# Optimization experiments

Hardware: AMD Instinct MI355X
Metric: run time of the kernel (lower is better)

Reference implementation:

```python
import jax, jax.numpy as jnp
import numpy as np

BATCH = 64
ORIGINAL_DIM = 524288
PROJ_DIM = 8192
C = 4


def setup_inputs() -> dict:
    key = jax.random.key(0)
    k1, k2, k3 = jax.random.split(key, 3)
    x = jax.random.normal(k1, (BATCH, ORIGINAL_DIM), dtype=jnp.float32)
    rand_indices = jax.random.randint(k2, (ORIGINAL_DIM, C), 0, PROJ_DIM, dtype=jnp.int32)
    rand_signs = jax.random.randint(k3, (ORIGINAL_DIM, C), 0, 2, dtype=jnp.int32)
    return {"x": x, "rand_indices": rand_indices, "rand_signs": rand_signs}


def reference(x, rand_indices, rand_signs):
    # SJLT: out[b, rand_indices[d, j]] += x[b, d] * sign[d, j], scaled by 1/sqrt(c)
    B, D = x.shape
    c = rand_indices.shape[1]
    signs = (2 * rand_signs - 1).astype(x.dtype)  # {0,1} -> {-1,+1}
    scale = 1.0 / jnp.sqrt(jnp.asarray(c, dtype=x.dtype))
    out = jnp.zeros((B, PROJ_DIM), dtype=x.dtype)
    for j in range(c):  # small fixed loop over non-zeros per column
        out = out.at[:, rand_indices[:, j]].add(x * signs[:, j])
    return out * scale
```

## Files before the change

### kernel.cpp

```cpp
#include <hip/hip_runtime.h>


constexpr int BATCH = 64;
constexpr int DIM   = 524288;
constexpr int PROJ  = 8192;
constexpr int NENT  = DIM * 4;
constexpr int CAP   = 384;
constexpr int CSTR  = 388;

constexpr int NBLKA = 256;
constexpr int EPB   = NENT / NBLKA;
constexpr int NHB   = 512;
constexpr int HBP   = PROJ / NHB;
constexpr int CAPH  = 4608;
constexpr int TBLK  = 2048;
constexpr int MAXR  = 5;

__device__ __forceinline__ uint32_t f2bf(float f) {
    uint32_t u = __float_as_uint(f);
    return (u + 0x7fffu + ((u >> 16) & 1u)) >> 16;
}

__global__ __launch_bounds__(1024) void prep_kernel(
    const float* __restrict__ x, const int4* __restrict__ idx4,
    const int4* __restrict__ sgn4, uint32_t* __restrict__ gBase,
    uint32_t* __restrict__ dense, uint32_t* __restrict__ xT)
{
    __shared__ uint32_t sh[10260];
    const int t = threadIdx.x;

    if (blockIdx.x < NBLKA) {
        uint32_t* cntL    = sh;
        uint32_t* offL    = sh + 512;
        uint32_t* curL    = sh + 1024;
        uint32_t* wsum    = sh + 1536;
        uint32_t* gb      = sh + 1544;
        uint32_t* staging = sh + 2056;
        const int lane = t & 63;
        const int blk  = blockIdx.x;

        if (t < NHB) cntL[t] = 0;
        __syncthreads();

        int4 iv[2], sv[2];
        int  dd[2];
#pragma unroll
        for (int j = 0; j < 2; ++j) {
            int d = blk * 2048 + j * 1024 + t;
            dd[j] = d;
            iv[j] = idx4[d];
            sv[j] = sgn4[d];
        }
#pragma unroll
        for (int j = 0; j < 2; ++j) {
            atomicAdd(&cntL[(uint32_t)iv[j].x >> 4], 1u);
            atomicAdd(&cntL[(uint32_t)iv[j].y >> 4], 1u);
            atomicAdd(&cntL[(uint32_t)iv[j].z >> 4], 1u);
            atomicAdd(&cntL[(uint32_t)iv[j].w >> 4], 1u);
        }
        __syncthreads();
        uint32_t v = 0, s = 0;
        if (t < NHB) {
            s = cntL[t]; v = s;
#pragma unroll
            for (int off = 1; off < 64; off <<= 1) {
                uint32_t u = __shfl_up(v, off);
                if (lane >= off) v += u;
            }
            if (lane == 63) wsum[t >> 6] = v;
        }
        __syncthreads();
        if (t < NHB) {
            uint32_t wb = 0;
            for (int w0 = 0; w0 < (t >> 6); ++w0) wb += wsum[w0];
            uint32_t ex = wb + v - s;
            offL[t] = ex;
            curL[t] = ex;
        }
        __syncthreads();
#pragma unroll
        for (int j = 0; j < 2; ++j) {
            const uint32_t dv = (uint32_t)dd[j] << 1;
            int p, ss;
            uint32_t b, sl;
            p = iv[j].x; ss = sv[j].x & 1; b = (uint32_t)p >> 4;
            sl = atomicAdd(&curL[b], 1u);
            staging[sl] = ((uint32_t)(p & 15) << 20) | dv | (uint32_t)ss;
            p = iv[j].y; ss = sv[j].y & 1; b = (uint32_t)p >> 4;
            sl = atomicAdd(&curL[b], 1u);
            staging[sl] = ((uint32_t)(p & 15) << 20) | dv | (uint32_t)ss;
            p = iv[j].z; ss = sv[j].z & 1; b = (uint32_t)p >> 4;
            sl = atomicAdd(&curL[b], 1u);
            staging[sl] = ((uint32_t)(p & 15) << 20) | dv | (uint32_t)ss;
            p = iv[j].w; ss = sv[j].w & 1; b = (uint32_t)p >> 4;
            sl = atomicAdd(&curL[b], 1u);
            staging[sl] = ((uint32_t)(p & 15) << 20) | dv | (uint32_t)ss;
        }
        __syncthreads();
        if (t < NHB) gb[t] = atomicAdd(&gBase[t], cntL[t]);
        __syncthreads();
        const int w = t >> 6;
        for (int i = 0; i < NHB / 16; ++i) {
            const int b = w * (NHB / 16) + i;
            const uint32_t c   = cntL[b];
            const uint32_t src = offL[b];
            const uint32_t g0  = gb[b];
            const uint32_t lim = (g0 < (uint32_t)CAPH) ? ((uint32_t)CAPH - g0) : 0u;
            const uint32_t cw  = c < lim ? c : lim;
            uint32_t* dst = dense + (size_t)b * CAPH + g0;
            for (uint32_t j2 = lane; j2 < cw; j2 += 64) dst[j2] = staging[src + j2];
        }
    } else {
        float* tile = reinterpret_cast<float*>(sh);
        const int blk   = blockIdx.x - NBLKA;
        const int dbase = blk * 256;
        const int c  = t & 15;
        const int r  = t >> 4;
        const int a  = t & 15;
        const int dr = t >> 4;
#pragma unroll
        for (int it = 0; it < 4; ++it) {
            const int d0 = dbase + it * 64;
            float4 v = *reinterpret_cast<const float4*>(
                &x[(size_t)r * DIM + d0 + 4 * c]);
            __syncthreads();
            tile[r * 65 + 4 * c + 0] = v.x;
            tile[r * 65 + 4 * c + 1] = v.y;
            tile[r * 65 + 4 * c + 2] = v.z;
            tile[r * 65 + 4 * c + 3] = v.w;
            __syncthreads();
            uint32_t lo, hi;
            lo = f2bf(tile[(4 * a + 0) * 65 + dr] * 0.5f);
            hi = f2bf(tile[(4 * a + 1) * 65 + dr] * 0.5f);
            const uint32_t w0 = lo | (hi << 16);
            lo = f2bf(tile[(4 * a + 2) * 65 + dr] * 0.5f);
            hi = f2bf(tile[(4 * a + 3) * 65 + dr] * 0.5f);
            const uint32_t w1 = lo | (hi << 16);
            uint2 wv; wv.x = w0; wv.y = w1;
            *reinterpret_cast<uint2*>(&xT[(size_t)(d0 + dr) * 32 + 2 * a]) = wv;
        }
    }
}

__global__ __launch_bounds__(1024) void gather8_kernel(
    const uint32_t* __restrict__ dense, const uint32_t* __restrict__ gBase,
    const uint32_t* __restrict__ xT, float* __restrict__ out)
{
    __shared__ uint32_t csr[16 * CSTR];
    __shared__ uint32_t wcnt[16][16];
    __shared__ uint32_t baseL[16][16];
    __shared__ uint32_t cntF[16];
    __shared__ float    obuf[64][17];
    const int t    = threadIdx.x;
    const int w    = t >> 6;
    const int lane = t & 63;
    const int hb   = blockIdx.x;

    uint32_t nt = gBase[hb];
    if (nt > (uint32_t)CAPH) nt = (uint32_t)CAPH;
    const uint32_t* src = dense + (size_t)hb * CAPH;
    const uint32_t s0 = (nt * (uint32_t)w) >> 4;
    const uint32_t s1 = (nt * (uint32_t)(w + 1)) >> 4;

    uint32_t pay[MAXR];
    uint32_t c16[16];
#pragma unroll
    for (int q = 0; q < 16; ++q) c16[q] = 0;
#pragma unroll
    for (int r = 0; r < MAXR; ++r) {
        const uint32_t i2 = s0 + (uint32_t)(r * 64 + lane);
        const bool ok = i2 < s1;
        pay[r] = ok ? src[i2] : 0xFFFFFFFFu;
        const uint32_t pv = ok ? ((pay[r] >> 20) & 15u) : 99u;
#pragma unroll
        for (int q = 0; q < 16; ++q) {
            const unsigned long long m = __ballot(pv == (uint32_t)q);
            c16[q] += (uint32_t)__popcll(m);
        }
    }
    if (lane == 0) {
#pragma unroll
        for (int q = 0; q < 16; ++q) wcnt[w][q] = c16[q];
    }
    __syncthreads();
    if (t < 256) {
        const int w2 = t >> 4, q2 = t & 15;
        uint32_t acc = 0;
        for (int wp = 0; wp < w2; ++wp) acc += wcnt[wp][q2];
        baseL[w2][q2] = (uint32_t)(q2 * CSTR) + acc;
        if (w2 == 15) cntF[q2] = acc + wcnt[15][q2];
    }
    __syncthreads();
    uint32_t rb[16];
#pragma unroll
    for (int q = 0; q < 16; ++q) rb[q] = baseL[w][q];
    const unsigned long long below = ((unsigned long long)1 << lane) - 1ull;
#pragma unroll
    for (int r = 0; r < MAXR; ++r) {
        const uint32_t i2 = s0 + (uint32_t)(r * 64 + lane);
        const bool ok = i2 < s1;
        const uint32_t pv = ok ? ((pay[r] >> 20) & 15u) : 99u;
        uint32_t slot = 0xFFFFFFFFu;
#pragma unroll
        for (int q = 0; q < 16; ++q) {
            const unsigned long long m = __ballot(pv == (uint32_t)q);
            if (pv == (uint32_t)q) slot = rb[q] + (uint32_t)__popcll(m & below);
            rb[q] += (uint32_t)__popcll(m);
        }
        if (slot < (uint32_t)(16 * CSTR)) csr[slot] = pay[r] & 0xFFFFFu;
    }
    __syncthreads();

    const int half = lane >> 5;
    const int k    = lane & 31;
    const uint32_t n = cntF[w];
    const uint32_t* e = &csr[w * CSTR];
    float acc0 = 0.f, acc1 = 0.f;
    uint32_t base = 0;
    for (; base + 8 <= n; base += 8) {
        uint32_t e8[8];
#pragma unroll
        for (int q = 0; q < 8; ++q) e8[q] = e[base + q];
#pragma unroll
        for (int q = 0; q < 8; q += 2) {
            uint32_t sel = half ? e8[q + 1] : e8[q];
            uint32_t u = xT[(size_t)(sel >> 1) * 32 + k];
            u ^= (sel & 1u) ? 0u : 0x80008000u;
            acc0 += __uint_as_float(u << 16);
            acc1 += __uint_as_float(u & 0xffff0000u);
        }
    }
    for (; base < n; base += 2) {
        uint32_t eA = e[base];
        uint32_t eB = (base + 1 < n) ? e[base + 1] : 0u;
        uint32_t sel   = half ? eB : eA;
        bool     valid = (base + (uint32_t)half) < n;
        uint32_t u = 0u;
        if (valid) {
            u = xT[(size_t)(sel >> 1) * 32 + k];
            u ^= (sel & 1u) ? 0u : 0x80008000u;
        }
        acc0 += __uint_as_float(u << 16);
        acc1 += __uint_as_float(u & 0xffff0000u);
    }
    acc0 += __shfl_xor(acc0, 32);
    acc1 += __shfl_xor(acc1, 32);
    if (half == 0) {
        obuf[2 * k + 0][w] = acc0;
        obuf[2 * k + 1][w] = acc1;
    }
    __syncthreads();
    if (t < 256) {
        const int b = t >> 2, q = t & 3;
        float4 vv;
        vv.x = obuf[b][4 * q + 0];
        vv.y = obuf[b][4 * q + 1];
        vv.z = obuf[b][4 * q + 2];
        vv.w = obuf[b][4 * q + 3];
        *reinterpret_cast<float4*>(
            &out[(size_t)b * PROJ + hb * HBP + 4 * q]) = vv;
    }
}

__device__ __forceinline__ void lds_fadd(uint32_t byte_addr, float v) {
    asm volatile("ds_add_f32 %0, %1" :: "v"(byte_addr), "v"(v) : "memory");
}
__device__ __forceinline__ void lds_fadd_off32k(uint32_t byte_addr, float v) {
    asm volatile("ds_add_f32 %0, %1 offset:32768" :: "v"(byte_addr), "v"(v) : "memory");
}

__global__ __launch_bounds__(1024) void sjlt_scatter(
    const float* __restrict__ x, const int4* __restrict__ idx4,
    const int4* __restrict__ sgn4, float* __restrict__ out)
{
    __shared__ float acc[4 * PROJ];
    for (int i = threadIdx.x; i < 4 * PROJ; i += 1024) acc[i] = 0.0f;
    __syncthreads();
    const int row0 = blockIdx.y * 4;
    const int dbeg = blockIdx.x * (DIM / 16);
    const uint32_t accBase = (uint32_t)(uintptr_t)(&acc[0]);
    const float* xr0 = x + (size_t)(row0 + 0) * DIM;
    const float* xr1 = x + (size_t)(row0 + 1) * DIM;
    const float* xr2 = x + (size_t)(row0 + 2) * DIM;
    const float* xr3 = x + (size_t)(row0 + 3) * DIM;
    for (int d = dbeg + (int)threadIdx.x; d < dbeg + DIM / 16; d += 1024) {
        const int4 iv = idx4[d];
        const int4 sv = sgn4[d];
        const uint32_t u0 = __float_as_uint(xr0[d]);
        const uint32_t u1 = __float_as_uint(xr1[d]);
        const uint32_t u2 = __float_as_uint(xr2[d]);
        const uint32_t u3 = __float_as_uint(xr3[d]);
        const int p[4] = {iv.x, iv.y, iv.z, iv.w};
        const int s[4] = {sv.x, sv.y, sv.z, sv.w};
#pragma unroll
        for (int j = 0; j < 4; ++j) {
            const uint32_t flip = (uint32_t)(s[j] ^ 1) << 31;
            const uint32_t a01  = accBase + ((uint32_t)p[j] << 2);
            const uint32_t a23  = a01 + 2u * 32768u;
            lds_fadd        (a01, __uint_as_float(u0 ^ flip));
            lds_fadd_off32k (a01, __uint_as_float(u1 ^ flip));
            lds_fadd        (a23, __uint_as_float(u2 ^ flip));
            lds_fadd_off32k (a23, __uint_as_float(u3 ^ flip));
        }
    }
    __syncthreads();
    for (int i = threadIdx.x; i < 4 * PROJ; i += 1024) {
        const int r  = i >> 13;
        const int pp = i & (PROJ - 1);
        unsafeAtomicAdd(&out[(size_t)(row0 + r) * PROJ + pp], acc[i] * 0.5f);
    }
}

extern "C" void kernel_launch(void* const* d_in, const int* in_sizes, int n_in,
                              void* d_out, int out_size, void* d_ws, size_t ws_size,
                              hipStream_t stream) {
    const float* x   = (const float*)d_in[0];
    const int4*  idx = (const int4*) d_in[1];
    const int4*  sgn = (const int4*) d_in[2];
    float*       out = (float*)d_out;

    const size_t need_r13 = ((size_t)NHB + (size_t)NHB * CAPH + (size_t)DIM * 32) * 4;

    if (ws_size >= need_r13) {
        uint32_t* gBase = (uint32_t*)d_ws;
        uint32_t* dense = gBase + NHB;
        uint32_t* xT    = dense + (size_t)NHB * CAPH;

        hipMemsetAsync(gBase, 0, NHB * sizeof(uint32_t), stream);
        prep_kernel   <<<NBLKA + TBLK, 1024, 0, stream>>>(
            x, idx, sgn, gBase, dense, xT);
        gather8_kernel<<<NHB,          1024, 0, stream>>>(dense, gBase, xT, out);
    } else {
        hipMemsetAsync(d_out, 0, (size_t)out_size * sizeof(float), stream);
        dim3 grid(16, 16);
        sjlt_scatter<<<grid, 1024, 0, stream>>>(x, idx, sgn, out);
    }
}
```

Measured before the change: 309.9 us.

## Replace in-block CSR bucketing with per-wave register accumulators and tree reduction

The gather kernel no longer sorts each block's entries into 16 per-column CSR buckets in LDS using ballots and prefix sums. Each wave now walks its own slice of entries directly and adds every value into one of 16 register accumulators, picked by a wave-uniform switch on the column id. The waves' partial sums are then combined with a log-depth tree reduction through LDS. This removes the two ballot passes and the CSR build, but uses many more registers, runs half the lanes idle, and adds several barrier rounds for the reduction. It also relies on every entry a wave reads in one step having the same column id, since readfirstlane takes the first lane's value.

```diff
diff --git a/kernel.cpp b/kernel.cpp
--- a/kernel.cpp
+++ b/kernel.cpp
@@ -5,16 +5,12 @@
 constexpr int DIM   = 524288;
 constexpr int PROJ  = 8192;
 constexpr int NENT  = DIM * 4;
-constexpr int CAP   = 384;
-constexpr int CSTR  = 388;
-
 constexpr int NBLKA = 256;
 constexpr int EPB   = NENT / NBLKA;
 constexpr int NHB   = 512;
 constexpr int HBP   = PROJ / NHB;
 constexpr int CAPH  = 4608;
 constexpr int TBLK  = 2048;
-constexpr int MAXR  = 5;
 
 __device__ __forceinline__ uint32_t f2bf(float f) {
     uint32_t u = __float_as_uint(f);
@@ -142,123 +138,94 @@
     }
 }
 
-__global__ __launch_bounds__(1024) void gather8_kernel(
+#define G9_CASE(Q) case Q: acc0[Q] += v0; acc1[Q] += v1; break;
+#define G9_SWITCH(PV)                                                     \
+    switch (PV) {                                                         \
+        G9_CASE(0)  G9_CASE(1)  G9_CASE(2)  G9_CASE(3)                    \
+        G9_CASE(4)  G9_CASE(5)  G9_CASE(6)  G9_CASE(7)                    \
+        G9_CASE(8)  G9_CASE(9)  G9_CASE(10) G9_CASE(11)                   \
+        G9_CASE(12) G9_CASE(13) G9_CASE(14) G9_CASE(15)                   \
+        default: break;                                                   \
+    }
+
+__global__ __launch_bounds__(1024) void gather9_kernel(
     const uint32_t* __restrict__ dense, const uint32_t* __restrict__ gBase,
     const uint32_t* __restrict__ xT, float* __restrict__ out)
 {
-    __shared__ uint32_t csr[16 * CSTR];
-    __shared__ uint32_t wcnt[16][16];
-    __shared__ uint32_t baseL[16][16];
-    __shared__ uint32_t cntF[16];
-    __shared__ float    obuf[64][17];
+    __shared__ float2 red2[8 * 528];
     const int t    = threadIdx.x;
     const int w    = t >> 6;
     const int lane = t & 63;
+    const int k    = lane & 31;
     const int hb   = blockIdx.x;
 
     uint32_t nt = gBase[hb];
     if (nt > (uint32_t)CAPH) nt = (uint32_t)CAPH;
-    const uint32_t* src = dense + (size_t)hb * CAPH;
+    const uint32_t* seg = dense + (size_t)hb * CAPH;
     const uint32_t s0 = (nt * (uint32_t)w) >> 4;
     const uint32_t s1 = (nt * (uint32_t)(w + 1)) >> 4;
 
-    uint32_t pay[MAXR];
-    uint32_t c16[16];
-#pragma unroll
-    for (int q = 0; q < 16; ++q) c16[q] = 0;
-#pragma unroll
-    for (int r = 0; r < MAXR; ++r) {
-        const uint32_t i2 = s0 + (uint32_t)(r * 64 + lane);
-        const bool ok = i2 < s1;
-        pay[r] = ok ? src[i2] : 0xFFFFFFFFu;
-        const uint32_t pv = ok ? ((pay[r] >> 20) & 15u) : 99u;
-#pragma unroll
-        for (int q = 0; q < 16; ++q) {
-            const unsigned long long m = __ballot(pv == (uint32_t)q);
-            c16[q] += (uint32_t)__popcll(m);
-        }
-    }
-    if (lane == 0) {
-#pragma unroll
-        for (int q = 0; q < 16; ++q) wcnt[w][q] = c16[q];
+    float acc0[16], acc1[16];
+#pragma unroll
+    for (int q = 0; q < 16; ++q) { acc0[q] = 0.f; acc1[q] = 0.f; }
+
+    uint32_t base = s0;
+    for (; base + 8 <= s1; base += 8) {
+        uint32_t e8[8];
+#pragma unroll
+        for (int j = 0; j < 8; ++j) e8[j] = seg[base + j];
+        uint32_t u8[8];
+#pragma unroll
+        for (int j = 0; j < 8; ++j)
+            u8[j] = xT[(size_t)((e8[j] >> 1) & 0x7FFFFu) * 32 + k];
+#pragma unroll
+        for (int j = 0; j < 8; ++j) {
+            const uint32_t u = u8[j] ^ ((e8[j] & 1u) ? 0u : 0x80008000u);
+            const float v0 = __uint_as_float(u << 16);
+            const float v1 = __uint_as_float(u & 0xffff0000u);
+            const int pv = __builtin_amdgcn_readfirstlane((int)((e8[j] >> 20) & 15u));
+            G9_SWITCH(pv)
+        }
+    }
+    for (; base < s1; ++base) {
+        const uint32_t e = seg[base];
+        uint32_t u = xT[(size_t)((e >> 1) & 0x7FFFFu) * 32 + k];
+        u ^= (e & 1u) ? 0u : 0x80008000u;
+        const float v0 = __uint_as_float(u << 16);
+        const float v1 = __uint_as_float(u & 0xffff0000u);
+        const int pv = __builtin_amdgcn_readfirstlane((int)((e >> 20) & 15u));
+        G9_SWITCH(pv)
+    }
+
+#pragma unroll
+    for (int stride = 8; stride >= 1; stride >>= 1) {
+        if (w >= stride && w < 2 * stride && lane < 32) {
+            float2* dst = red2 + (w - stride) * 528;
+#pragma unroll
+            for (int q = 0; q < 16; ++q)
+                dst[q * 33 + k] = make_float2(acc0[q], acc1[q]);
+        }
+        __syncthreads();
+        if (w < stride && lane < 32) {
+            const float2* src = red2 + w * 528;
+#pragma unroll
+            for (int q = 0; q < 16; ++q) {
+                float2 v = src[q * 33 + k];
+                acc0[q] += v.x; acc1[q] += v.y;
+            }
+        }
+        __syncthreads();
+    }
+    if (w == 0 && lane < 32) {
+#pragma unroll
+        for (int q = 0; q < 16; ++q)
+            red2[q * 33 + k] = make_float2(acc0[q], acc1[q]);
     }
     __syncthreads();
-    if (t < 256) {
-        const int w2 = t >> 4, q2 = t & 15;
-        uint32_t acc = 0;
-        for (int wp = 0; wp < w2; ++wp) acc += wcnt[wp][q2];
-        baseL[w2][q2] = (uint32_t)(q2 * CSTR) + acc;
-        if (w2 == 15) cntF[q2] = acc + wcnt[15][q2];
-    }
-    __syncthreads();
-    uint32_t rb[16];
-#pragma unroll
-    for (int q = 0; q < 16; ++q) rb[q] = baseL[w][q];
-    const unsigned long long below = ((unsigned long long)1 << lane) - 1ull;
-#pragma unroll
-    for (int r = 0; r < MAXR; ++r) {
-        const uint32_t i2 = s0 + (uint32_t)(r * 64 + lane);
-        const bool ok = i2 < s1;
-        const uint32_t pv = ok ? ((pay[r] >> 20) & 15u) : 99u;
-        uint32_t slot = 0xFFFFFFFFu;
-#pragma unroll
-        for (int q = 0; q < 16; ++q) {
-            const unsigned long long m = __ballot(pv == (uint32_t)q);
-            if (pv == (uint32_t)q) slot = rb[q] + (uint32_t)__popcll(m & below);
-            rb[q] += (uint32_t)__popcll(m);
-        }
-        if (slot < (uint32_t)(16 * CSTR)) csr[slot] = pay[r] & 0xFFFFFu;
-    }
-    __syncthreads();
-
-    const int half = lane >> 5;
-    const int k    = lane & 31;
-    const uint32_t n = cntF[w];
-    const uint32_t* e = &csr[w * CSTR];
-    float acc0 = 0.f, acc1 = 0.f;
-    uint32_t base = 0;
-    for (; base + 8 <= n; base += 8) {
-        uint32_t e8[8];
-#pragma unroll
-        for (int q = 0; q < 8; ++q) e8[q] = e[base + q];
-#pragma unroll
-        for (int q = 0; q < 8; q += 2) {
-            uint32_t sel = half ? e8[q + 1] : e8[q];
-            uint32_t u = xT[(size_t)(sel >> 1) * 32 + k];
-            u ^= (sel & 1u) ? 0u : 0x80008000u;
-            acc0 += __uint_as_float(u << 16);
-            acc1 += __uint_as_float(u & 0xffff0000u);
-        }
-    }
-    for (; base < n; base += 2) {
-        uint32_t eA = e[base];
-        uint32_t eB = (base + 1 < n) ? e[base + 1] : 0u;
-        uint32_t sel   = half ? eB : eA;
-        bool     valid = (base + (uint32_t)half) < n;
-        uint32_t u = 0u;
-        if (valid) {
-            u = xT[(size_t)(sel >> 1) * 32 + k];
-            u ^= (sel & 1u) ? 0u : 0x80008000u;
-        }
-        acc0 += __uint_as_float(u << 16);
-        acc1 += __uint_as_float(u & 0xffff0000u);
-    }
-    acc0 += __shfl_xor(acc0, 32);
-    acc1 += __shfl_xor(acc1, 32);
-    if (half == 0) {
-        obuf[2 * k + 0][w] = acc0;
-        obuf[2 * k + 1][w] = acc1;
-    }
-    __syncthreads();
-    if (t < 256) {
-        const int b = t >> 2, q = t & 3;
-        float4 vv;
-        vv.x = obuf[b][4 * q + 0];
-        vv.y = obuf[b][4 * q + 1];
-        vv.z = obuf[b][4 * q + 2];
-        vv.w = obuf[b][4 * q + 3];
-        *reinterpret_cast<float4*>(
-            &out[(size_t)b * PROJ + hb * HBP + 4 * q]) = vv;
+    {
+        const int b = t >> 4, q = t & 15;
+        const float2 vq = red2[q * 33 + (b >> 1)];
+        out[(size_t)b * PROJ + hb * HBP + q] = (b & 1) ? vq.y : vq.x;
     }
 }
 
@@ -319,9 +286,9 @@
     const int4*  sgn = (const int4*) d_in[2];
     float*       out = (float*)d_out;
 
-    const size_t need_r13 = ((size_t)NHB + (size_t)NHB * CAPH + (size_t)DIM * 32) * 4;
-
-    if (ws_size >= need_r13) {
+    const size_t need = ((size_t)NHB + (size_t)NHB * CAPH + (size_t)DIM * 32) * 4;
+
+    if (ws_size >= need) {
         uint32_t* gBase = (uint32_t*)d_ws;
         uint32_t* dense = gBase + NHB;
         uint32_t* xT    = dense + (size_t)NHB * CAPH;
@@ -329,7 +296,7 @@
         hipMemsetAsync(gBase, 0, NHB * sizeof(uint32_t), stream);
         prep_kernel   <<<NBLKA + TBLK, 1024, 0, stream>>>(
             x, idx, sgn, gBase, dense, xT);
-        gather8_kernel<<<NHB,          1024, 0, stream>>>(dense, gBase, xT, out);
+        gather9_kernel<<<NHB,          1024, 0, stream>>>(dense, gBase, xT, out);
     } else {
         hipMemsetAsync(d_out, 0, (size_t)out_size * sizeof(float), stream);
         dim3 grid(16, 16);
```

Result: faster. 295.9 us (-4.5%).
